# Optimization experiments

Hardware: AMD Instinct MI355X
Metric: run time of the kernel (lower is better)

The kernel has to match this reference:

```python
import jax, jax.numpy as jnp
import numpy as np

T, D, DL, E, I, SI = 2048, 2048, 1024, 64, 768, 4096
TOP_K, N_GROUP, TOPK_GROUP = 6, 8, 4
ROUTED_SCALE = 2.5
CAP = 384


def relu2(x):
    r = jnp.maximum(x, 0.0)
    return r * r


def setup_inputs() -> dict:
    key = jax.random.key(0)
    ks = jax.random.split(key, 9)
    return {
        "hidden_states": jax.random.normal(ks[0], (T, D), jnp.float32),
        "gate_w": jax.random.normal(ks[1], (E, D), jnp.float32) * 0.02,
        "gate_bias": jax.random.normal(ks[2], (E,), jnp.float32) * 0.01,  # e_score_correction_bias
        "fc1_w": jax.random.normal(ks[3], (DL, D), jnp.float32) * 0.02,
        "fc2_w": jax.random.normal(ks[4], (D, DL), jnp.float32) * 0.02,
        "w1": jax.random.normal(ks[5], (E, I, DL), jnp.float32) * 0.02,
        "w2": jax.random.normal(ks[6], (E, DL, I), jnp.float32) * 0.02,
        "sw1": jax.random.normal(ks[7], (SI, D), jnp.float32) * 0.02,
        "sw2": jax.random.normal(ks[8], (D, SI), jnp.float32) * 0.02,
    }


def reference(hidden_states, gate_w, gate_bias, fc1_w, fc2_w, w1, w2, sw1, sw2):
    x = hidden_states  # [T, D]
    # ---- DeepseekV3-style gate (sigmoid + bias-corrected group top-k) ----
    logits = x.astype(jnp.float32) @ gate_w.T.astype(jnp.float32)  # [T, E]
    scores = jax.nn.sigmoid(logits)
    sb = scores + gate_bias  # selection scores with correction bias
    gsb = sb.reshape(T, N_GROUP, E // N_GROUP)
    group_scores = jax.lax.top_k(gsb, 2)[0].sum(-1)  # [T, G] = sum of top-2 per group
    _, gidx = jax.lax.top_k(group_scores, TOPK_GROUP)
    gmask = jax.nn.one_hot(gidx, N_GROUP, dtype=sb.dtype).sum(1)  # [T, G]
    emask = jnp.repeat(gmask, E // N_GROUP, axis=1)  # [T, E]
    masked = jnp.where(emask > 0, sb, 0.0)
    _, tidx = jax.lax.top_k(masked, TOP_K)  # [T, K] selected expert ids
    tw = jnp.take_along_axis(scores, tidx, axis=1)  # weights from un-biased scores
    tw = tw / (tw.sum(-1, keepdims=True) + 1e-20) * ROUTED_SCALE  # [T, K]
    # ---- latent down-projection (fc1_latent_proj) ----
    xl = x @ fc1_w.T  # [T, DL]
    # ---- dispatch to per-expert buffers ----
    flat_e = tidx.reshape(-1)                 # [T*K]
    tok = jnp.repeat(jnp.arange(T), TOP_K)    # [T*K]
    oh = jax.nn.one_hot(flat_e, E, dtype=jnp.int32)              # [T*K, E]
    pos = jnp.sum((jnp.cumsum(oh, axis=0) - 1) * oh, axis=1)     # slot within expert
    valid = pos < CAP
    pos_c = jnp.where(valid, pos, 0)
    buf = jnp.zeros((E, CAP, DL), xl.dtype)
    buf = buf.at[flat_e, pos_c].add(jnp.where(valid[:, None], xl[tok], 0.0))
    # ---- grouped expert FFN: fc2(relu(fc1(x))^2) ----
    h = relu2(jnp.einsum('ecd,eid->eci', buf, w1))  # [E, CAP, I]
    out = jnp.einsum('eci,edi->ecd', h, w2)         # [E, CAP, DL]
    # ---- combine with routing weights ----
    gathered = out[flat_e, pos_c] * valid[:, None].astype(out.dtype)  # [T*K, DL]
    routed = jnp.sum(gathered.reshape(T, TOP_K, DL) * tw[..., None].astype(out.dtype), axis=1)
    routed = routed @ fc2_w.T  # fc2_latent_proj, [T, D]
    # ---- shared experts (relu2 MLP) run in parallel ----
    shared = relu2(x @ sw1.T) @ sw2.T  # [T, D]
    return shared + routed
```

## Files before the change

### kernel.cpp

```cpp
#include <hip/hip_runtime.h>

typedef unsigned int u32;
typedef unsigned short u16;
typedef __attribute__((ext_vector_type(4))) float floatx4;
typedef __attribute__((ext_vector_type(8))) __bf16 bf16x8;

#define T_ 2048
#define D_ 2048
#define DL_ 1024
#define E_ 64
#define I_ 768
#define SI_ 4096
#define TOPK 6
#define NGRP 8
#define TOPG 4
#define CAP_ 384

#define BM 128
#define BK 32

__device__ __forceinline__ u16 f2bf(float f) {
  u32 u = __builtin_bit_cast(u32, f);
  u += 0x7fffu + ((u >> 16) & 1u);
  return (u16)(u >> 16);
}
__device__ __forceinline__ float bf2f(u16 h) {
  return __builtin_bit_cast(float, ((u32)h) << 16);
}

__device__ __forceinline__ void async16(const u16* g, u16* l) {
  __builtin_amdgcn_global_load_lds((const __attribute__((address_space(1))) void*)g,
                                   (__attribute__((address_space(3))) void*)l, 16, 0, 0);
}

__global__ __launch_bounds__(256) void cvt_f2b_k(const float* __restrict__ src,
                                                 u16* __restrict__ dst, int n8) {
  int i = blockIdx.x * 256 + threadIdx.x;
  if (i >= n8) return;
  const float4* s4 = (const float4*)src;
  float4 a = s4[2 * i], b = s4[2 * i + 1];
  u32 p0 = (u32)f2bf(a.x) | ((u32)f2bf(a.y) << 16);
  u32 p1 = (u32)f2bf(a.z) | ((u32)f2bf(a.w) << 16);
  u32 p2 = (u32)f2bf(b.x) | ((u32)f2bf(b.y) << 16);
  u32 p3 = (u32)f2bf(b.z) | ((u32)f2bf(b.w) << 16);
  ((uint4*)dst)[i] = make_uint4(p0, p1, p2, p3);
}

__global__ __launch_bounds__(256) void gate_logits_k(const float* __restrict__ x,
                                                     const float* __restrict__ gw,
                                                     float* __restrict__ logits) {
  __shared__ float xs[16 * 65];
  __shared__ float wsd[32 * 65];
  const int tid = threadIdx.x;
  const int t0 = blockIdx.x * 16;
  const int e0 = blockIdx.y * 32;
  const int tl = tid & 15, eb = (tid >> 4) * 2;
  const int xr = tid >> 4, xc = (tid & 15) * 4;
  const int wr = tid >> 3, wc = (tid & 7) * 8;
  float acc[2] = {0.f, 0.f};
  for (int kc = 0; kc < D_; kc += 64) {
    __syncthreads();
    float4 xv = *(const float4*)&x[(size_t)(t0 + xr) * D_ + kc + xc];
    xs[xr * 65 + xc + 0] = xv.x;
    xs[xr * 65 + xc + 1] = xv.y;
    xs[xr * 65 + xc + 2] = xv.z;
    xs[xr * 65 + xc + 3] = xv.w;
#pragma unroll
    for (int i = 0; i < 2; ++i) {
      float4 wv = *(const float4*)&gw[(size_t)(e0 + wr) * D_ + kc + wc + i * 4];
      wsd[wr * 65 + wc + i * 4 + 0] = wv.x;
      wsd[wr * 65 + wc + i * 4 + 1] = wv.y;
      wsd[wr * 65 + wc + i * 4 + 2] = wv.z;
      wsd[wr * 65 + wc + i * 4 + 3] = wv.w;
    }
    __syncthreads();
#pragma unroll 4
    for (int kk = 0; kk < 64; ++kk) {
      float xvv = xs[tl * 65 + kk];
      acc[0] += xvv * wsd[eb * 65 + kk];
      acc[1] += xvv * wsd[(eb + 1) * 65 + kk];
    }
  }
  logits[(size_t)(t0 + tl) * E_ + e0 + eb + 0] = acc[0];
  logits[(size_t)(t0 + tl) * E_ + e0 + eb + 1] = acc[1];
}

__global__ __launch_bounds__(256) void route_k(const float* __restrict__ logits,
                                               const float* __restrict__ bias,
                                               int* __restrict__ cnts,
                                               int* __restrict__ etok,
                                               int* __restrict__ row_of,
                                               float* __restrict__ tww) {
  const int wid = threadIdx.x >> 6, lane = threadIdx.x & 63;
  const int t = blockIdx.x * 4 + wid;
  float lg = logits[(size_t)t * E_ + lane];
  float s = 1.f / (1.f + __expf(-lg));
  float sb = s + bias[lane];
  const int g = lane >> 3;
  float m1 = sb;
  m1 = fmaxf(m1, __shfl_xor(m1, 1));
  m1 = fmaxf(m1, __shfl_xor(m1, 2));
  m1 = fmaxf(m1, __shfl_xor(m1, 4));
  unsigned long long b1 = __ballot(sb == m1);
  int am = __ffsll((unsigned long long)((b1 >> (g * 8)) & 0xFFull)) - 1 + g * 8;
  float v2 = (lane == am) ? -1e30f : sb;
  float m2 = v2;
  m2 = fmaxf(m2, __shfl_xor(m2, 1));
  m2 = fmaxf(m2, __shfl_xor(m2, 2));
  m2 = fmaxf(m2, __shfl_xor(m2, 4));
  float gs = m1 + m2;
  float gsv[NGRP];
#pragma unroll
  for (int gg = 0; gg < NGRP; ++gg) gsv[gg] = __shfl(gs, gg * 8);
  unsigned selm = 0;
#pragma unroll
  for (int r = 0; r < TOPG; ++r) {
    float best = -1e30f; int bi = 0;
#pragma unroll
    for (int gg = 0; gg < NGRP; ++gg)
      if (!((selm >> gg) & 1) && gsv[gg] > best) { best = gsv[gg]; bi = gg; }
    selm |= 1u << bi;
  }
  float val = ((selm >> g) & 1) ? sb : 0.0f;
  float wsum = 0.f; int selr = -1;
#pragma unroll
  for (int r = 0; r < TOPK; ++r) {
    float m = val;
    m = fmaxf(m, __shfl_xor(m, 1));
    m = fmaxf(m, __shfl_xor(m, 2));
    m = fmaxf(m, __shfl_xor(m, 4));
    m = fmaxf(m, __shfl_xor(m, 8));
    m = fmaxf(m, __shfl_xor(m, 16));
    m = fmaxf(m, __shfl_xor(m, 32));
    unsigned long long b2 = __ballot(val == m);
    int am2 = __ffsll(b2) - 1;
    if (lane == am2) { selr = r; val = -1e30f; }
    wsum += __shfl(s, am2);
  }
  float inv = 2.5f / (wsum + 1e-20f);
  if (selr >= 0) {
    int slot = atomicAdd(&cnts[lane], 1);
    int rowid = -1;
    if (slot < CAP_) { rowid = lane * CAP_ + slot; etok[rowid] = t; }
    row_of[t * TOPK + selr] = rowid;
    tww[t * TOPK + selr] = s * inv;
  }
}

template <int EPI, bool GATHER, int BNT>
__global__ __launch_bounds__(256) void gemm_bf(const u16* __restrict__ A,
                                               const u16* __restrict__ B,
                                               void* __restrict__ Cp,
                                               int M, int K, int ldA, int ldB, int ldC,
                                               long sAe, long sBe, long sCe,
                                               const int* __restrict__ counts,
                                               const int* __restrict__ gather) {
  constexpr int NJ = BNT / 32;
  __shared__ u16 As[2][BM * BK];
  __shared__ u16 Bs[2][BNT * BK];
  const int e = blockIdx.z;
  int Mloc = M;
  if (counts) { Mloc = counts[e]; if (Mloc > CAP_) Mloc = CAP_; }
  const int m0 = blockIdx.y * BM;
  if (m0 >= Mloc) return;
  const int n0 = blockIdx.x * BNT;
  const int tid = threadIdx.x;
  const int wave = tid >> 6, lane = tid & 63;
  const int lrow = lane >> 2;
  const int lcol = (lane & 3) * 8;

  int ar0 = m0 + wave * 32 + lrow;
  int ar1 = ar0 + 16;
  const u16 *aS0, *aS1, *bS0, *bS1 = nullptr;
  if (GATHER) {
    int t0i = (ar0 < Mloc) ? gather[e * CAP_ + ar0] : 0;
    int t1i = (ar1 < Mloc) ? gather[e * CAP_ + ar1] : 0;
    aS0 = A + (size_t)t0i * ldA + lcol;
    aS1 = A + (size_t)t1i * ldA + lcol;
  } else {
    aS0 = A + (size_t)e * sAe + (size_t)ar0 * ldA + lcol;
    aS1 = A + (size_t)e * sAe + (size_t)ar1 * ldA + lcol;
  }
  if (BNT == 128) {
    int br0 = n0 + wave * 32 + lrow;
    bS0 = B + (size_t)e * sBe + (size_t)br0 * ldB + lcol;
    bS1 = B + (size_t)e * sBe + (size_t)(br0 + 16) * ldB + lcol;
  } else {
    int br0 = n0 + wave * 16 + lrow;
    bS0 = B + (size_t)e * sBe + (size_t)br0 * ldB + lcol;
  }

  auto issue = [&](int kt, int p) {
    async16(aS0 + kt, &As[p][(wave * 32 + 0) * BK]);
    async16(aS1 + kt, &As[p][(wave * 32 + 16) * BK]);
    if (BNT == 128) {
      async16(bS0 + kt, &Bs[p][(wave * 32 + 0) * BK]);
      async16(bS1 + kt, &Bs[p][(wave * 32 + 16) * BK]);
    } else {
      async16(bS0 + kt, &Bs[p][(wave * 16) * BK]);
    }
  };

  floatx4 acc[4][NJ];
#pragma unroll
  for (int i = 0; i < 4; ++i)
#pragma unroll
    for (int j = 0; j < NJ; ++j) acc[i][j] = floatx4{0.f, 0.f, 0.f, 0.f};

  const int wm = (wave & 1) * 64;
  const int wn = (wave >> 1) * (BNT == 128 ? 64 : 32);
  const int lr = lane & 15, lk = (lane >> 4) * 8;

  issue(0, 0);
  int p = 0;
  for (int kt = 0; kt < K; kt += BK, p ^= 1) {
    __syncthreads();
    if (kt + BK < K) issue(kt + BK, p ^ 1);
    bf16x8 af[4], bfr[NJ];
#pragma unroll
    for (int i = 0; i < 4; ++i)
      af[i] = *(const bf16x8*)&As[p][(wm + i * 16 + lr) * BK + lk];
#pragma unroll
    for (int j = 0; j < NJ; ++j)
      bfr[j] = *(const bf16x8*)&Bs[p][(wn + j * 16 + lr) * BK + lk];
#pragma unroll
    for (int i = 0; i < 4; ++i)
#pragma unroll
      for (int j = 0; j < NJ; ++j)
        acc[i][j] = __builtin_amdgcn_mfma_f32_16x16x32_bf16(af[i], bfr[j], acc[i][j], 0, 0, 0);
  }

  const int rbase = (lane >> 4) * 4;
#pragma unroll
  for (int i = 0; i < 4; ++i) {
#pragma unroll
    for (int r = 0; r < 4; ++r) {
      int grow = m0 + wm + i * 16 + rbase + r;
      if (grow >= Mloc) continue;
      size_t crow = (size_t)sCe * e + (size_t)grow * ldC;
#pragma unroll
      for (int j = 0; j < NJ; ++j) {
        int gcol = n0 + wn + j * 16 + lr;
        float v = acc[i][j][r];
        if constexpr (EPI == 0) {
          ((u16*)Cp)[crow + gcol] = f2bf(v);
        } else if constexpr (EPI == 1) {
          v = fmaxf(v, 0.f); v *= v;
          ((u16*)Cp)[crow + gcol] = f2bf(v);
        } else if constexpr (EPI == 2) {
          ((float*)Cp)[crow + gcol] = v;
        } else {
          ((float*)Cp)[crow + gcol] += v;
        }
      }
    }
  }
}

#define LDS_PAD 40
#define BNF 128
template <int ATYPE, int EPI>
__global__ __launch_bounds__(256, 2) void gemm_nt(const void* __restrict__ Ap,
                                                  const float* __restrict__ Bp,
                                                  void* __restrict__ Cp,
                                                  int M, int K, int ldA, int ldB, int ldC,
                                                  long sAe, long sBe, long sCe,
                                                  const int* __restrict__ counts,
                                                  const int* __restrict__ gather) {
  __shared__ u16 As[BM * LDS_PAD];
  __shared__ u16 Bs[BNF * LDS_PAD];
  const int e = blockIdx.z;
  int Mloc = M;
  if (counts) { Mloc = counts[e]; if (Mloc > CAP_) Mloc = CAP_; }
  const int m0 = blockIdx.y * BM;
  if (m0 >= Mloc) return;
  const int n0 = blockIdx.x * BNF;
  const int tid = threadIdx.x;
  const int row = tid >> 1;
  const int colb = (tid & 1) * 16;
  const int arow = m0 + row;
  int arowIdx;
  if (gather) arowIdx = (arow < Mloc) ? gather[e * CAP_ + arow] : 0;
  else arowIdx = arow;
  const float* Af32 = (const float*)Ap + (size_t)e * sAe + (size_t)arowIdx * ldA;
  const u16* Abf = (const u16*)Ap + (size_t)e * sAe + (size_t)arowIdx * ldA;
  const float* Brow = Bp + (size_t)e * sBe + (size_t)(n0 + row) * ldB;
  float4 ra[4]; uint4 rab[2]; float4 rb[4];
  auto loadAB = [&](int kt) {
    if constexpr (ATYPE == 0) {
#pragma unroll
      for (int i = 0; i < 4; ++i) ra[i] = *(const float4*)&Af32[kt + colb + i * 4];
    } else {
#pragma unroll
      for (int i = 0; i < 2; ++i) rab[i] = *(const uint4*)&Abf[kt + colb + i * 8];
    }
#pragma unroll
    for (int i = 0; i < 4; ++i) rb[i] = *(const float4*)&Brow[kt + colb + i * 4];
  };
  auto stage = [&]() {
    uint4* ad = (uint4*)&As[row * LDS_PAD + colb];
    if constexpr (ATYPE == 0) {
      u32 w[8];
#pragma unroll
      for (int i = 0; i < 4; ++i) {
        w[2 * i] = (u32)f2bf(ra[i].x) | ((u32)f2bf(ra[i].y) << 16);
        w[2 * i + 1] = (u32)f2bf(ra[i].z) | ((u32)f2bf(ra[i].w) << 16);
      }
      ad[0] = make_uint4(w[0], w[1], w[2], w[3]);
      ad[1] = make_uint4(w[4], w[5], w[6], w[7]);
    } else {
      ad[0] = rab[0]; ad[1] = rab[1];
    }
    u32 wb[8];
#pragma unroll
    for (int i = 0; i < 4; ++i) {
      wb[2 * i] = (u32)f2bf(rb[i].x) | ((u32)f2bf(rb[i].y) << 16);
      wb[2 * i + 1] = (u32)f2bf(rb[i].z) | ((u32)f2bf(rb[i].w) << 16);
    }
    uint4* bd = (uint4*)&Bs[row * LDS_PAD + colb];
    bd[0] = make_uint4(wb[0], wb[1], wb[2], wb[3]);
    bd[1] = make_uint4(wb[4], wb[5], wb[6], wb[7]);
  };
  floatx4 acc[4][4];
#pragma unroll
  for (int i = 0; i < 4; ++i)
#pragma unroll
    for (int j = 0; j < 4; ++j) acc[i][j] = floatx4{0.f, 0.f, 0.f, 0.f};
  const int wave = tid >> 6, lane = tid & 63;
  const int wm = (wave & 1) * 64, wn = (wave >> 1) * 64;
  const int lr = lane & 15, lk = (lane >> 4) * 8;
  loadAB(0);
  for (int kt = 0; kt < K; kt += BK) {
    __syncthreads();
    stage();
    __syncthreads();
    if (kt + BK < K) loadAB(kt + BK);
    bf16x8 af[4], bfr[4];
#pragma unroll
    for (int i = 0; i < 4; ++i)
      af[i] = *(const bf16x8*)&As[(wm + i * 16 + lr) * LDS_PAD + lk];
#pragma unroll
    for (int j = 0; j < 4; ++j)
      bfr[j] = *(const bf16x8*)&Bs[(wn + j * 16 + lr) * LDS_PAD + lk];
#pragma unroll
    for (int i = 0; i < 4; ++i)
#pragma unroll
      for (int j = 0; j < 4; ++j)
        acc[i][j] = __builtin_amdgcn_mfma_f32_16x16x32_bf16(af[i], bfr[j], acc[i][j], 0, 0, 0);
  }
  const int rbase = (lane >> 4) * 4;
#pragma unroll
  for (int i = 0; i < 4; ++i) {
#pragma unroll
    for (int r = 0; r < 4; ++r) {
      int grow = m0 + wm + i * 16 + rbase + r;
      if (grow >= Mloc) continue;
      size_t crow = (size_t)sCe * e + (size_t)grow * ldC;
#pragma unroll
      for (int j = 0; j < 4; ++j) {
        int gcol = n0 + wn + j * 16 + lr;
        float v = acc[i][j][r];
        if constexpr (EPI == 0) {
          ((u16*)Cp)[crow + gcol] = f2bf(v);
        } else if constexpr (EPI == 1) {
          v = fmaxf(v, 0.f); v *= v;
          ((u16*)Cp)[crow + gcol] = f2bf(v);
        } else if constexpr (EPI == 2) {
          ((float*)Cp)[crow + gcol] = v;
        } else {
          ((float*)Cp)[crow + gcol] += v;
        }
      }
    }
  }
}

__global__ __launch_bounds__(256) void combine_k(const u16* __restrict__ eout,
                                                 const int* __restrict__ row_of,
                                                 const float* __restrict__ tww,
                                                 u16* __restrict__ ylat) {
  int t = blockIdx.x;
  int c0 = threadIdx.x * 4;
  float a0 = 0.f, a1 = 0.f, a2 = 0.f, a3 = 0.f;
#pragma unroll
  for (int k = 0; k < TOPK; ++k) {
    int r = row_of[t * TOPK + k];
    float w = tww[t * TOPK + k];
    if (r >= 0) {
      uint2 v = *(const uint2*)&eout[(size_t)r * DL_ + c0];
      a0 += w * bf2f((u16)(v.x & 0xffffu));
      a1 += w * bf2f((u16)(v.x >> 16));
      a2 += w * bf2f((u16)(v.y & 0xffffu));
      a3 += w * bf2f((u16)(v.y >> 16));
    }
  }
  u32 o0 = (u32)f2bf(a0) | ((u32)f2bf(a1) << 16);
  u32 o1 = (u32)f2bf(a2) | ((u32)f2bf(a3) << 16);
  *(uint2*)&ylat[(size_t)t * DL_ + c0] = make_uint2(o0, o1);
}

extern "C" void kernel_launch(void* const* d_in, const int* in_sizes, int n_in,
                              void* d_out, int out_size, void* d_ws, size_t ws_size,
                              hipStream_t stream) {
  (void)in_sizes; (void)n_in; (void)out_size;
  const float* x = (const float*)d_in[0];
  const float* gw = (const float*)d_in[1];
  const float* gbias = (const float*)d_in[2];
  const float* fc1 = (const float*)d_in[3];
  const float* fc2 = (const float*)d_in[4];
  const float* w1 = (const float*)d_in[5];
  const float* w2 = (const float*)d_in[6];
  const float* sw1 = (const float*)d_in[7];
  const float* sw2 = (const float*)d_in[8];
  float* out = (float*)d_out;

  char* ws = (char*)d_ws;
  size_t off = 0;
  auto alloc = [&](size_t bytes) {
    char* p = ws + off;
    off += (bytes + 255) & ~(size_t)255;
    return p;
  };
  float* logits = (float*)alloc((size_t)T_ * E_ * 4);
  int* cnts = (int*)alloc(E_ * 4);
  int* etok = (int*)alloc((size_t)E_ * CAP_ * 4);
  int* row_of = (int*)alloc((size_t)T_ * TOPK * 4);
  float* tww = (float*)alloc((size_t)T_ * TOPK * 4);
  u16* xl = (u16*)alloc((size_t)T_ * DL_ * 2);
  u16* ylat = (u16*)alloc((size_t)T_ * DL_ * 2);

  size_t big1_elems = (size_t)E_ * CAP_ * I_;
  if ((size_t)T_ * SI_ > big1_elems) big1_elems = (size_t)T_ * SI_;
  size_t need_fast = off + (((size_t)T_ * D_ * 2 + 255) & ~255ul)
                     + (((size_t)D_ * DL_ * 2 + 255) & ~255ul)
                     + ((big1_elems * 2 + 255) & ~255ul)
                     + (((size_t)E_ * CAP_ * DL_ * 2 + 255) & ~255ul)
                     + (((size_t)E_ * I_ * DL_ * 2 + 255) & ~255ul);

  hipMemsetAsync(cnts, 0, E_ * 4, stream);
  gate_logits_k<<<dim3(T_ / 16, 2), 256, 0, stream>>>(x, gw, logits);
  route_k<<<T_ / 4, 256, 0, stream>>>(logits, gbias, cnts, etok, row_of, tww);

  if (ws_size >= need_fast) {
    u16* xbf = (u16*)alloc((size_t)T_ * D_ * 2);
    u16* fc2b = (u16*)alloc((size_t)D_ * DL_ * 2);
    u16* big1 = (u16*)alloc(big1_elems * 2);
    u16* eoutB = (u16*)alloc((size_t)E_ * CAP_ * DL_ * 2);
    u16* wbuf = (u16*)alloc((size_t)E_ * I_ * DL_ * 2);
    u16* sw1b = wbuf;
    u16* sw2b = wbuf + (size_t)SI_ * D_;
    u16* fc1b = wbuf + 2 * (size_t)SI_ * D_;

    cvt_f2b_k<<<(T_ * D_ / 8 + 255) / 256, 256, 0, stream>>>(x, xbf, T_ * D_ / 8);
    cvt_f2b_k<<<(SI_ * D_ / 8 + 255) / 256, 256, 0, stream>>>(sw1, sw1b, SI_ * D_ / 8);
    cvt_f2b_k<<<(SI_ * D_ / 8 + 255) / 256, 256, 0, stream>>>(sw2, sw2b, SI_ * D_ / 8);
    cvt_f2b_k<<<(DL_ * D_ / 8 + 255) / 256, 256, 0, stream>>>(fc1, fc1b, DL_ * D_ / 8);
    cvt_f2b_k<<<(D_ * DL_ / 8 + 255) / 256, 256, 0, stream>>>(fc2, fc2b, D_ * DL_ / 8);

    gemm_bf<1, false, 128><<<dim3(SI_ / 128, T_ / BM, 1), 256, 0, stream>>>(
        xbf, sw1b, big1, T_, D_, D_, D_, SI_, 0, 0, 0, nullptr, nullptr);
    gemm_bf<2, false, 64><<<dim3(D_ / 64, T_ / BM, 1), 256, 0, stream>>>(
        big1, sw2b, out, T_, SI_, SI_, SI_, D_, 0, 0, 0, nullptr, nullptr);

    gemm_bf<0, false, 64><<<dim3(DL_ / 64, T_ / BM, 1), 256, 0, stream>>>(
        xbf, fc1b, xl, T_, D_, D_, D_, DL_, 0, 0, 0, nullptr, nullptr);

    int nw = E_ * I_ * DL_ / 8;
    cvt_f2b_k<<<(nw + 255) / 256, 256, 0, stream>>>(w1, wbuf, nw);
    gemm_bf<1, true, 128><<<dim3(I_ / 128, CAP_ / BM, E_), 256, 0, stream>>>(
        xl, wbuf, big1, CAP_, DL_, DL_, DL_, I_,
        0, (long)I_ * DL_, (long)CAP_ * I_, cnts, etok);

    cvt_f2b_k<<<(nw + 255) / 256, 256, 0, stream>>>(w2, wbuf, nw);
    gemm_bf<0, false, 128><<<dim3(DL_ / 128, CAP_ / BM, E_), 256, 0, stream>>>(
        big1, wbuf, eoutB, CAP_, I_, I_, I_, DL_,
        (long)CAP_ * I_, (long)DL_ * I_, (long)CAP_ * DL_, cnts, nullptr);

    combine_k<<<T_, 256, 0, stream>>>(eoutB, row_of, tww, ylat);

    gemm_bf<3, false, 64><<<dim3(D_ / 64, T_ / BM, 1), 256, 0, stream>>>(
        ylat, fc2b, out, T_, DL_, DL_, DL_, D_, 0, 0, 0, nullptr, nullptr);
  } else {
    char* big = alloc((size_t)E_ * CAP_ * I_ * 2 + (size_t)E_ * CAP_ * DL_ * 2);
    u16* hs = (u16*)big;
    u16* h = (u16*)big;
    u16* eoutB = (u16*)(big + (size_t)E_ * CAP_ * I_ * 2);

    gemm_nt<0, 1><<<dim3(SI_ / BNF, T_ / BM, 1), 256, 0, stream>>>(
        x, sw1, hs, T_, D_, D_, D_, SI_, 0, 0, 0, nullptr, nullptr);
    gemm_nt<1, 2><<<dim3(D_ / BNF, T_ / BM, 1), 256, 0, stream>>>(
        hs, sw2, out, T_, SI_, SI_, SI_, D_, 0, 0, 0, nullptr, nullptr);
    gemm_nt<0, 0><<<dim3(DL_ / BNF, T_ / BM, 1), 256, 0, stream>>>(
        x, fc1, xl, T_, D_, D_, D_, DL_, 0, 0, 0, nullptr, nullptr);
    gemm_nt<1, 1><<<dim3(I_ / BNF, CAP_ / BM, E_), 256, 0, stream>>>(
        xl, w1, h, CAP_, DL_, DL_, DL_, I_,
        0, (long)I_ * DL_, (long)CAP_ * I_, cnts, etok);
    gemm_nt<1, 0><<<dim3(DL_ / BNF, CAP_ / BM, E_), 256, 0, stream>>>(
        h, w2, eoutB, CAP_, I_, I_, I_, DL_,
        (long)CAP_ * I_, (long)DL_ * I_, (long)CAP_ * DL_, cnts, nullptr);
    combine_k<<<T_, 256, 0, stream>>>(eoutB, row_of, tww, ylat);
    gemm_nt<1, 3><<<dim3(D_ / BNF, T_ / BM, 1), 256, 0, stream>>>(
        ylat, fc2, out, T_, DL_, DL_, DL_, D_, 0, 0, 0, nullptr, nullptr);
  }
}
```

Baseline: 884.1 us.

## Convert fp32 weights to bf16 inside GEMM loads and fuse sw1/fc1 GEMMs

Drops the separate fp32-to-bf16 conversion kernels for the weights. The GEMM now loads fp32 weight tiles into registers, converts them, and writes bf16 into LDS, software-pipelined across two buffers. The shared-expert up-projection and the fc1 latent projection are merged into one launch that picks B and C per column block. Epilogues go through LDS for coalesced vector stores. This removes the extra weight read/write passes and a launch, but doubles B global load bytes inside the GEMM and puts conversion work in the main loop.

Result: slower. 942.3 us (+6.6%).

```diff
diff --git a/kernel.cpp b/kernel.cpp
--- a/kernel.cpp
+++ b/kernel.cpp
@@ -147,17 +147,21 @@
   }
 }
 
-template <int EPI, bool GATHER, int BNT>
-__global__ __launch_bounds__(256) void gemm_bf(const u16* __restrict__ A,
-                                               const u16* __restrict__ B,
-                                               void* __restrict__ Cp,
-                                               int M, int K, int ldA, int ldB, int ldC,
-                                               long sAe, long sBe, long sCe,
-                                               const int* __restrict__ counts,
-                                               const int* __restrict__ gather) {
+template <int BNT, int EPI, bool GATHER, bool FUSED>
+__global__ __launch_bounds__(256) void gemm_bw(
+    const u16* __restrict__ A, const float* __restrict__ B0, void* __restrict__ C0,
+    int M, int K, int ldA, int ldB, int ldC0,
+    long sAe, long sBe, long sCe,
+    const int* __restrict__ counts, const int* __restrict__ gather,
+    int nsplit, const float* __restrict__ B2, void* __restrict__ C2, int ldC2) {
   constexpr int NJ = BNT / 32;
-  __shared__ u16 As[2][BM * BK];
-  __shared__ u16 Bs[2][BNT * BK];
+  constexpr int EPT = BNT * BK / 256;
+  constexpr int NF4 = EPT / 4;
+  constexpr int TPR = BK / EPT;
+  __shared__ u16 smem[16384];
+  u16* AsB = smem;
+  u16* BsB = smem + 2 * BM * BK;
+
   const int e = blockIdx.z;
   int Mloc = M;
   if (counts) { Mloc = counts[e]; if (Mloc > CAP_) Mloc = CAP_; }
@@ -166,12 +170,10 @@
   const int n0 = blockIdx.x * BNT;
   const int tid = threadIdx.x;
   const int wave = tid >> 6, lane = tid & 63;
-  const int lrow = lane >> 2;
-  const int lcol = (lane & 3) * 8;
-
-  int ar0 = m0 + wave * 32 + lrow;
-  int ar1 = ar0 + 16;
-  const u16 *aS0, *aS1, *bS0, *bS1 = nullptr;
+  const int lrow = lane >> 2, lcol = (lane & 3) * 8;
+
+  int ar0 = m0 + wave * 32 + lrow, ar1 = ar0 + 16;
+  const u16 *aS0, *aS1;
   if (GATHER) {
     int t0i = (ar0 < Mloc) ? gather[e * CAP_ + ar0] : 0;
     int t1i = (ar1 < Mloc) ? gather[e * CAP_ + ar1] : 0;
@@ -181,24 +183,38 @@
     aS0 = A + (size_t)e * sAe + (size_t)ar0 * ldA + lcol;
     aS1 = A + (size_t)e * sAe + (size_t)ar1 * ldA + lcol;
   }
-  if (BNT == 128) {
-    int br0 = n0 + wave * 32 + lrow;
-    bS0 = B + (size_t)e * sBe + (size_t)br0 * ldB + lcol;
-    bS1 = B + (size_t)e * sBe + (size_t)(br0 + 16) * ldB + lcol;
+  const float* Bsel;
+  int n0loc = n0;
+  if (FUSED) {
+    if (n0 < nsplit) { Bsel = B0; } else { Bsel = B2; n0loc = n0 - nsplit; }
   } else {
-    int br0 = n0 + wave * 16 + lrow;
-    bS0 = B + (size_t)e * sBe + (size_t)br0 * ldB + lcol;
-  }
-
-  auto issue = [&](int kt, int p) {
-    async16(aS0 + kt, &As[p][(wave * 32 + 0) * BK]);
-    async16(aS1 + kt, &As[p][(wave * 32 + 16) * BK]);
-    if (BNT == 128) {
-      async16(bS0 + kt, &Bs[p][(wave * 32 + 0) * BK]);
-      async16(bS1 + kt, &Bs[p][(wave * 32 + 16) * BK]);
-    } else {
-      async16(bS0 + kt, &Bs[p][(wave * 16) * BK]);
-    }
+    Bsel = B0 + (size_t)e * sBe;
+  }
+  const int brow = tid / TPR;
+  const int bkc = (tid % TPR) * EPT;
+  const float* Bln = Bsel + (size_t)(n0loc + brow) * ldB + bkc;
+
+  auto issueA = [&](int kt, int p) {
+    u16* base = AsB + p * (BM * BK);
+    async16(aS0 + kt, base + (wave * 32 + 0) * BK);
+    async16(aS1 + kt, base + (wave * 32 + 16) * BK);
+  };
+  float4 rA[NF4], rB[NF4];
+  auto loadB = [&](int kt, float4* r) {
+#pragma unroll
+    for (int f = 0; f < NF4; ++f) r[f] = *(const float4*)(Bln + kt + f * 4);
+  };
+  auto writeB = [&](const float4* r, int p) {
+    u32 w[EPT / 2];
+#pragma unroll
+    for (int f = 0; f < NF4; ++f) {
+      w[2 * f]     = (u32)f2bf(r[f].x) | ((u32)f2bf(r[f].y) << 16);
+      w[2 * f + 1] = (u32)f2bf(r[f].z) | ((u32)f2bf(r[f].w) << 16);
+    }
+    uint4* dst = (uint4*)(BsB + p * (BNT * BK) + brow * BK + bkc);
+#pragma unroll
+    for (int f = 0; f < NF4 / 2; ++f)
+      dst[f] = make_uint4(w[4 * f], w[4 * f + 1], w[4 * f + 2], w[4 * f + 3]);
   };
 
   floatx4 acc[4][NJ];
@@ -208,50 +224,93 @@
     for (int j = 0; j < NJ; ++j) acc[i][j] = floatx4{0.f, 0.f, 0.f, 0.f};
 
   const int wm = (wave & 1) * 64;
-  const int wn = (wave >> 1) * (BNT == 128 ? 64 : 32);
+  const int wn = (wave >> 1) * (NJ * 16);
   const int lr = lane & 15, lk = (lane >> 4) * 8;
 
-  issue(0, 0);
-  int p = 0;
-  for (int kt = 0; kt < K; kt += BK, p ^= 1) {
-    __syncthreads();
-    if (kt + BK < K) issue(kt + BK, p ^ 1);
+  auto compute = [&](int p) {
+    const u16* Ab = AsB + p * (BM * BK);
+    const u16* Bb = BsB + p * (BNT * BK);
     bf16x8 af[4], bfr[NJ];
 #pragma unroll
     for (int i = 0; i < 4; ++i)
-      af[i] = *(const bf16x8*)&As[p][(wm + i * 16 + lr) * BK + lk];
+      af[i] = *(const bf16x8*)&Ab[(wm + i * 16 + lr) * BK + lk];
 #pragma unroll
     for (int j = 0; j < NJ; ++j)
-      bfr[j] = *(const bf16x8*)&Bs[p][(wn + j * 16 + lr) * BK + lk];
+      bfr[j] = *(const bf16x8*)&Bb[(wn + j * 16 + lr) * BK + lk];
 #pragma unroll
     for (int i = 0; i < 4; ++i)
 #pragma unroll
       for (int j = 0; j < NJ; ++j)
         acc[i][j] = __builtin_amdgcn_mfma_f32_16x16x32_bf16(af[i], bfr[j], acc[i][j], 0, 0, 0);
-  }
-
+  };
+
+  loadB(0, rA);
+  writeB(rA, 0);
+  issueA(0, 0);
+  loadB(BK, rB);
+  for (int kt = 0; kt < K; kt += 2 * BK) {
+    __syncthreads();
+    if (kt + BK < K) { issueA(kt + BK, 1); writeB(rB, 1); }
+    if (kt + 2 * BK < K) loadB(kt + 2 * BK, rA);
+    compute(0);
+    __syncthreads();
+    if (kt + 2 * BK < K) { issueA(kt + 2 * BK, 0); writeB(rA, 0); }
+    if (kt + 3 * BK < K) loadB(kt + 3 * BK, rB);
+    compute(1);
+  }
+
+  __syncthreads();
   const int rbase = (lane >> 4) * 4;
-#pragma unroll
-  for (int i = 0; i < 4; ++i) {
-#pragma unroll
-    for (int r = 0; r < 4; ++r) {
-      int grow = m0 + wm + i * 16 + rbase + r;
-      if (grow >= Mloc) continue;
-      size_t crow = (size_t)sCe * e + (size_t)grow * ldC;
-#pragma unroll
-      for (int j = 0; j < NJ; ++j) {
-        int gcol = n0 + wn + j * 16 + lr;
-        float v = acc[i][j][r];
-        if constexpr (EPI == 0) {
-          ((u16*)Cp)[crow + gcol] = f2bf(v);
-        } else if constexpr (EPI == 1) {
-          v = fmaxf(v, 0.f); v *= v;
-          ((u16*)Cp)[crow + gcol] = f2bf(v);
-        } else if constexpr (EPI == 2) {
-          ((float*)Cp)[crow + gcol] = v;
-        } else {
-          ((float*)Cp)[crow + gcol] += v;
+  if constexpr (EPI <= 1) {
+    bool doRelu = (EPI == 1);
+    void* Cq = C0; int ldC = ldC0; int nc0 = n0;
+    if (FUSED) {
+      if (n0 < nsplit) { doRelu = true; }
+      else { Cq = C2; ldC = ldC2; nc0 = n0 - nsplit; doRelu = false; }
+    }
+    u16* Cs = smem;
+#pragma unroll
+    for (int i = 0; i < 4; ++i)
+#pragma unroll
+      for (int r = 0; r < 4; ++r)
+#pragma unroll
+        for (int j = 0; j < NJ; ++j) {
+          float v = acc[i][j][r];
+          if (doRelu) { v = fmaxf(v, 0.f); v *= v; }
+          Cs[(wm + i * 16 + rbase + r) * BNT + wn + j * 16 + lr] = f2bf(v);
         }
+    __syncthreads();
+    const int srow = tid >> 1, sc0 = (tid & 1) * (BNT / 2);
+    if (m0 + srow < Mloc) {
+      u16* gdst = (u16*)Cq + (size_t)sCe * e + (size_t)(m0 + srow) * ldC + nc0 + sc0;
+      const u16* ssrc = Cs + srow * BNT + sc0;
+#pragma unroll
+      for (int q = 0; q < BNT / 16; ++q)
+        ((uint4*)gdst)[q] = ((const uint4*)ssrc)[q];
+    }
+  } else {
+    static_assert(BNT == 64 || EPI <= 1, "fp32 bounce needs BNT=64");
+    float* Cs = (float*)smem;
+#pragma unroll
+    for (int i = 0; i < 4; ++i)
+#pragma unroll
+      for (int r = 0; r < 4; ++r)
+#pragma unroll
+        for (int j = 0; j < NJ; ++j)
+          Cs[(wm + i * 16 + rbase + r) * BNT + wn + j * 16 + lr] = acc[i][j][r];
+    __syncthreads();
+    const int srow = tid >> 1, sc0 = (tid & 1) * (BNT / 2);
+    if (m0 + srow < Mloc) {
+      float* gdst = (float*)C0 + (size_t)(m0 + srow) * ldC0 + n0 + sc0;
+      const float* ssrc = Cs + srow * BNT + sc0;
+#pragma unroll
+      for (int q = 0; q < BNT / 8; ++q) {
+        float4 v = ((const float4*)ssrc)[q];
+        if constexpr (EPI == 3) {
+          float4 o = ((const float4*)gdst)[q];
+          v.x += o.x; v.y += o.y; v.z += o.z; v.w += o.w;
+        }
+        ((float4*)gdst)[q] = v;
       }
     }
   }
@@ -432,10 +491,8 @@
   size_t big1_elems = (size_t)E_ * CAP_ * I_;
   if ((size_t)T_ * SI_ > big1_elems) big1_elems = (size_t)T_ * SI_;
   size_t need_fast = off + (((size_t)T_ * D_ * 2 + 255) & ~255ul)
-                     + (((size_t)D_ * DL_ * 2 + 255) & ~255ul)
                      + ((big1_elems * 2 + 255) & ~255ul)
-                     + (((size_t)E_ * CAP_ * DL_ * 2 + 255) & ~255ul)
-                     + (((size_t)E_ * I_ * DL_ * 2 + 255) & ~255ul);
+                     + (((size_t)E_ * CAP_ * DL_ * 2 + 255) & ~255ul);
 
   hipMemsetAsync(cnts, 0, E_ * 4, stream);
   gate_logits_k<<<dim3(T_ / 16, 2), 256, 0, stream>>>(x, gw, logits);
@@ -443,43 +500,32 @@
 
   if (ws_size >= need_fast) {
     u16* xbf = (u16*)alloc((size_t)T_ * D_ * 2);
-    u16* fc2b = (u16*)alloc((size_t)D_ * DL_ * 2);
     u16* big1 = (u16*)alloc(big1_elems * 2);
     u16* eoutB = (u16*)alloc((size_t)E_ * CAP_ * DL_ * 2);
-    u16* wbuf = (u16*)alloc((size_t)E_ * I_ * DL_ * 2);
-    u16* sw1b = wbuf;
-    u16* sw2b = wbuf + (size_t)SI_ * D_;
-    u16* fc1b = wbuf + 2 * (size_t)SI_ * D_;
 
     cvt_f2b_k<<<(T_ * D_ / 8 + 255) / 256, 256, 0, stream>>>(x, xbf, T_ * D_ / 8);
-    cvt_f2b_k<<<(SI_ * D_ / 8 + 255) / 256, 256, 0, stream>>>(sw1, sw1b, SI_ * D_ / 8);
-    cvt_f2b_k<<<(SI_ * D_ / 8 + 255) / 256, 256, 0, stream>>>(sw2, sw2b, SI_ * D_ / 8);
-    cvt_f2b_k<<<(DL_ * D_ / 8 + 255) / 256, 256, 0, stream>>>(fc1, fc1b, DL_ * D_ / 8);
-    cvt_f2b_k<<<(D_ * DL_ / 8 + 255) / 256, 256, 0, stream>>>(fc2, fc2b, D_ * DL_ / 8);
-
-    gemm_bf<1, false, 128><<<dim3(SI_ / 128, T_ / BM, 1), 256, 0, stream>>>(
-        xbf, sw1b, big1, T_, D_, D_, D_, SI_, 0, 0, 0, nullptr, nullptr);
-    gemm_bf<2, false, 64><<<dim3(D_ / 64, T_ / BM, 1), 256, 0, stream>>>(
-        big1, sw2b, out, T_, SI_, SI_, SI_, D_, 0, 0, 0, nullptr, nullptr);
-
-    gemm_bf<0, false, 64><<<dim3(DL_ / 64, T_ / BM, 1), 256, 0, stream>>>(
-        xbf, fc1b, xl, T_, D_, D_, D_, DL_, 0, 0, 0, nullptr, nullptr);
-
-    int nw = E_ * I_ * DL_ / 8;
-    cvt_f2b_k<<<(nw + 255) / 256, 256, 0, stream>>>(w1, wbuf, nw);
-    gemm_bf<1, true, 128><<<dim3(I_ / 128, CAP_ / BM, E_), 256, 0, stream>>>(
-        xl, wbuf, big1, CAP_, DL_, DL_, DL_, I_,
-        0, (long)I_ * DL_, (long)CAP_ * I_, cnts, etok);
-
-    cvt_f2b_k<<<(nw + 255) / 256, 256, 0, stream>>>(w2, wbuf, nw);
-    gemm_bf<0, false, 128><<<dim3(DL_ / 128, CAP_ / BM, E_), 256, 0, stream>>>(
-        big1, wbuf, eoutB, CAP_, I_, I_, I_, DL_,
-        (long)CAP_ * I_, (long)DL_ * I_, (long)CAP_ * DL_, cnts, nullptr);
+
+    gemm_bw<128, 1, false, true><<<dim3((SI_ + DL_) / 128, T_ / BM, 1), 256, 0, stream>>>(
+        xbf, sw1, big1, T_, D_, D_, D_, SI_, 0, 0, 0, nullptr, nullptr,
+        SI_, fc1, xl, DL_);
+
+    gemm_bw<64, 2, false, false><<<dim3(D_ / 64, T_ / BM, 1), 256, 0, stream>>>(
+        big1, sw2, out, T_, SI_, SI_, SI_, D_, 0, 0, 0, nullptr, nullptr,
+        0, nullptr, nullptr, 0);
+
+    gemm_bw<128, 1, true, false><<<dim3(I_ / 128, CAP_ / BM, E_), 256, 0, stream>>>(
+        xl, w1, big1, CAP_, DL_, DL_, DL_, I_,
+        0, (long)I_ * DL_, (long)CAP_ * I_, cnts, etok, 0, nullptr, nullptr, 0);
+
+    gemm_bw<128, 0, false, false><<<dim3(DL_ / 128, CAP_ / BM, E_), 256, 0, stream>>>(
+        big1, w2, eoutB, CAP_, I_, I_, I_, DL_,
+        (long)CAP_ * I_, (long)DL_ * I_, (long)CAP_ * DL_, cnts, nullptr, 0, nullptr, nullptr, 0);
 
     combine_k<<<T_, 256, 0, stream>>>(eoutB, row_of, tww, ylat);
 
-    gemm_bf<3, false, 64><<<dim3(D_ / 64, T_ / BM, 1), 256, 0, stream>>>(
-        ylat, fc2b, out, T_, DL_, DL_, DL_, D_, 0, 0, 0, nullptr, nullptr);
+    gemm_bw<64, 3, false, false><<<dim3(D_ / 64, T_ / BM, 1), 256, 0, stream>>>(
+        ylat, fc2, out, T_, DL_, DL_, DL_, D_, 0, 0, 0, nullptr, nullptr,
+        0, nullptr, nullptr, 0);
   } else {
     char* big = alloc((size_t)E_ * CAP_ * I_ * 2 + (size_t)E_ * CAP_ * DL_ * 2);
     u16* hs = (u16*)big;
```
